# Optimization experiments

Measured on AMD Instinct MI355X. Metric: run time of the kernel, lower is better.

Reference implementation:

```python
import jax, jax.numpy as jnp
import numpy as np

N_SAMPLES, N_ASSETS = 64, 256
N_CLUSTERS, N_INIT, MAX_ITER = 8, 10, 30
SEED = 42


def cov2corr(cov):
    d = jnp.sqrt(jnp.diagonal(cov, axis1=-2, axis2=-1))
    return cov / (d[..., :, None] * d[..., None, :])


def kmeans_single(x, key):
    # x: (n, d) points; Lloyd's algorithm, 'random' init (pick n_clusters points).
    n = x.shape[0]
    idx = jax.random.choice(key, n, (N_CLUSTERS,), replace=False)
    centers0 = x[idx]

    def step(centers, _):
        d2 = ((x[:, None, :] - centers[None, :, :]) ** 2).sum(-1)  # (n, k)
        ixs = jnp.argmin(d2, axis=1)
        onehot = jax.nn.one_hot(ixs, N_CLUSTERS, dtype=x.dtype)    # (n, k)
        counts = onehot.sum(0)
        new_centers = (onehot.T @ x) / jnp.maximum(counts, 1.0)[:, None]
        new_centers = jnp.where(counts[:, None] > 0, new_centers, centers)
        return new_centers, None

    centers, _ = jax.lax.scan(step, centers0, None, length=MAX_ITER)
    d2 = ((x[:, None, :] - centers[None, :, :]) ** 2).sum(-1)
    ixs = jnp.argmin(d2, axis=1)
    inertia = jnp.min(d2, axis=1).sum()
    return ixs, inertia


def cluster_weights(mask, cov, r):
    # Masked-block analytical Markowitz: solving the system with identity on the
    # off-cluster block and zero RHS is exactly the sub-matrix solve of the original.
    n = cov.shape[0]
    eye = jnp.eye(n, dtype=cov.dtype)
    m2 = mask[:, None] & mask[None, :]
    A = jnp.where(m2, cov, eye)
    b = jnp.where(mask, r, 0.0)
    w = jnp.linalg.solve(A, b)          # zeros outside cluster by construction
    denom = w.sum()                     # = ones^T Sigma_c^{-1} mu_c
    return jnp.where(denom != 0, w / denom, 0.0)


def nco_sample(cov, r, key):
    corr = cov2corr(cov)
    keys = jax.random.split(key, N_INIT)
    ixs_all, inertia = jax.vmap(lambda k: kmeans_single(corr, k))(keys)
    ixs = jax.lax.stop_gradient(ixs_all[jnp.argmin(inertia)])      # (n,)
    masks = ixs[None, :] == jnp.arange(N_CLUSTERS)[:, None]        # (k, n)
    w_cols = jax.vmap(cluster_weights, in_axes=(0, None, None))(masks, cov, r)  # (k, n)
    w_intra = w_cols.T                                             # (n, k)
    inter_cov = w_intra.T @ cov @ w_intra                          # (k, k)
    inter_rets = w_intra.T @ r                                     # (k,)
    w_u = jnp.linalg.solve(inter_cov, inter_rets)
    w_inter = w_u / w_u.sum()
    return w_intra @ w_inter                                       # (n,)


def setup_inputs() -> dict:
    key = jax.random.key(0)
    k1, k2 = jax.random.split(key)
    # SPD covariance: factor model + diagonal jitter
    F = jax.random.normal(k1, (N_SAMPLES, N_ASSETS, N_ASSETS), dtype=jnp.float32)
    covmat = jnp.einsum('bij,bkj->bik', F, F) / N_ASSETS \
        + 0.1 * jnp.eye(N_ASSETS, dtype=jnp.float32)[None]
    rets = jax.random.uniform(k2, (N_SAMPLES, N_ASSETS), dtype=jnp.float32,
                              minval=0.01, maxval=1.0)
    return {"covmat": covmat, "rets": rets}


def reference(covmat, rets):
    base = jax.random.key(SEED)
    keys = jax.random.split(base, covmat.shape[0])
    return jax.vmap(nco_sample)(covmat, rets, keys)  # (n_samples, n_assets)
```

## Files before the change

### kernel.cpp

```cpp
#include <hip/hip_runtime.h>
#include <stdint.h>

#define NS 64
#define NA 256
#define NC 8
#define NI 10
#define MAXIT 30
#define MSMALL 64
#define MLDS 132

typedef unsigned int u32;
typedef unsigned long long u64;

struct Key { u32 x, y; };

__device__ __forceinline__ void tf2x32(u32 k0, u32 k1, u32 c0, u32 c1, u32& o0, u32& o1) {
  u32 ks0 = k0, ks1 = k1, ks2 = k0 ^ k1 ^ 0x1BD11BDAu;
  u32 x0 = c0 + ks0, x1 = c1 + ks1;
#define TFR(r) { x0 += x1; x1 = (x1 << (r)) | (x1 >> (32 - (r))); x1 ^= x0; }
  TFR(13) TFR(15) TFR(26) TFR(6)
  x0 += ks1; x1 += ks2 + 1u;
  TFR(17) TFR(29) TFR(16) TFR(24)
  x0 += ks2; x1 += ks0 + 2u;
  TFR(13) TFR(15) TFR(26) TFR(6)
  x0 += ks0; x1 += ks1 + 3u;
  TFR(17) TFR(29) TFR(16) TFR(24)
  x0 += ks1; x1 += ks2 + 4u;
  TFR(13) TFR(15) TFR(26) TFR(6)
  x0 += ks2; x1 += ks0 + 5u;
#undef TFR
  o0 = x0; o1 = x1;
}

__device__ __forceinline__ Key key_row(Key k, u32 j) {
  Key r; tf2x32(k.x, k.y, 0u, j, r.x, r.y); return r;
}
__device__ __forceinline__ u32 rbits32(Key k, u32 i) {
  u32 o0, o1; tf2x32(k.x, k.y, 0u, i, o0, o1); return o0 ^ o1;
}

__global__ __launch_bounds__(256) void nco_gram_kernel(
    const float* __restrict__ cov, double* __restrict__ G) {
  int b = blockIdx.x;
  int j = b / 10, tile = b - 10 * j;
  const int TIa[10] = {0,0,0,0,1,1,1,2,2,3};
  const int TJa[10] = {0,1,2,3,1,2,3,2,3,3};
  int ti2 = TIa[tile], tj2 = TJa[tile];
  const float* C = cov + (size_t)j * NA * NA;
  double* Gj = G + (size_t)j * NA * NA;

  __shared__ double sinv[NA];
  __shared__ double As[16][64 + 1];
  __shared__ double Bs[16][64 + 1];
  int t = threadIdx.x;
  int tr = t >> 4, tc = t & 15;

  sinv[t] = 1.0 / sqrt((double)C[(size_t)t * NA + t]);
  __syncthreads();

  double acc[4][4];
#pragma unroll
  for (int a = 0; a < 4; a++)
#pragma unroll
    for (int bb = 0; bb < 4; bb++) acc[a][bb] = 0.0;

  for (int k0 = 0; k0 < NA; k0 += 16) {
    int kk = t & 15, rr = t >> 4;
    double ck = sinv[k0 + kk];
#pragma unroll
    for (int m = 0; m < 4; m++) {
      int r = rr + 16 * m;
      int gr = ti2 * 64 + r;
      As[kk][r] = (double)C[(size_t)gr * NA + k0 + kk] * sinv[gr] * ck;
      int gc = tj2 * 64 + r;
      Bs[kk][r] = (double)C[(size_t)gc * NA + k0 + kk] * sinv[gc] * ck;
    }
    __syncthreads();
#pragma unroll
    for (int kk2 = 0; kk2 < 16; kk2++) {
      double ar[4], br[4];
#pragma unroll
      for (int m = 0; m < 4; m++) ar[m] = As[kk2][tr + 16 * m];
#pragma unroll
      for (int m = 0; m < 4; m++) br[m] = Bs[kk2][tc + 16 * m];
#pragma unroll
      for (int a = 0; a < 4; a++)
#pragma unroll
        for (int bb = 0; bb < 4; bb++) acc[a][bb] = fma(ar[a], br[bb], acc[a][bb]);
    }
    __syncthreads();
  }
#pragma unroll
  for (int a = 0; a < 4; a++) {
    int gr = ti2 * 64 + tr + 16 * a;
#pragma unroll
    for (int bb = 0; bb < 4; bb++) {
      int gc = tj2 * 64 + tc + 16 * bb;
      Gj[(size_t)gr * NA + gc] = acc[a][bb];
      if (ti2 != tj2) Gj[(size_t)gc * NA + gr] = acc[a][bb];
    }
  }
}

__global__ __launch_bounds__(512) void nco_kmeans_kernel(
    const double* __restrict__ G, int* __restrict__ ixsAll,
    double* __restrict__ inertiaAll) {
  int b = blockIdx.x;
  int xcd = b & 7, s0 = b >> 3;
  int j  = xcd + 8 * (s0 / NI);
  int mi = s0 - (s0 / NI) * NI;
  int blk = j * NI + mi;
  int tid = threadIdx.x;
  int t = tid & 255;
  int g = tid >> 8;
  int w4 = tid >> 6;
  const double* Gj = G + (size_t)j * NA * NA;

  __shared__ int    li[NC][NA];
  __shared__ double sv[NC][NA];
  __shared__ int    wcnt[4][NC];
  __shared__ u64    balPrev[4][NC];
  __shared__ u64    balNew[4][NC];
  __shared__ u64    dAdd[4][NC];
  __shared__ u64    dRem[4][NC];
  __shared__ int    nsz[NC];
  __shared__ int    dirty[NC];
  __shared__ double part[NC][8];
  __shared__ double sinvn[NC], ck2[NC];
  __shared__ u32    bits[NA];

  if (g == 0) {
    Key base; base.x = 0u; base.y = 42u;
    Key skey = key_row(base, (u32)j);
    Key ikey = key_row(skey, (u32)mi);
    Key sub  = key_row(ikey, 1u);
    bits[t] = rbits32(sub, (u32)t);
  }
  __syncthreads();
  if (g == 0) {
    u32 mine = bits[t];
    int rank = 0;
    for (int u = 0; u < NA; u++) {
      u32 b2 = bits[u];
      rank += (b2 < mine) || (b2 == mine && u < t);
    }
    if (rank < NC) li[rank][0] = t;
    if (t < NC) { nsz[t] = 1; dirty[t] = 1; }
#pragma unroll
    for (int k = 0; k < NC; k++) {
      u64 bal = __ballot(rank == k);
      if ((t & 63) == 0) balPrev[w4][k] = bal;
    }
  }
  __syncthreads();

  double xx = (g == 0) ? Gj[(size_t)t * NA + t] : 0.0;
  int myix = -1;
  double fb = 0.0;
  for (int it = 0; it <= MAXIT; ++it) {
    if (it > 0) {
      u64 mybal = 0;
      if (g == 0) {
#pragma unroll
        for (int k = 0; k < NC; k++) {
          u64 bal = __ballot(myix == k);
          if ((t & 63) == 0) { wcnt[w4][k] = (int)__popcll(bal); balNew[w4][k] = bal; }
          if (k == myix) mybal = bal;
        }
      }
      __syncthreads();
      if (g == 0) {
        if (t < NC) {
          int tot = wcnt[0][t] + wcnt[1][t] + wcnt[2][t] + wcnt[3][t];
          if (tot > 0) {
            nsz[t] = tot;
            bool d = (balNew[0][t] != balPrev[0][t]) | (balNew[1][t] != balPrev[1][t]) |
                     (balNew[2][t] != balPrev[2][t]) | (balNew[3][t] != balPrev[3][t]);
            dirty[t] = d ? 1 : 0;
            if (d) {
#pragma unroll
              for (int w2 = 0; w2 < 4; w2++) {
                dAdd[w2][t] = balNew[w2][t] & ~balPrev[w2][t];
                dRem[w2][t] = balPrev[w2][t] & ~balNew[w2][t];
                balPrev[w2][t] = balNew[w2][t];
              }
            }
          } else {
            dirty[t] = 0;
          }
        }
        int k = myix;
        int base = 0;
        for (int w2 = 0; w2 < w4; w2++) base += wcnt[w2][k];
        li[k][base + (int)__popcll(mybal & ((1ULL << (t & 63)) - 1ULL))] = t;
      }
      __syncthreads();
      if (!(dirty[0] | dirty[1] | dirty[2] | dirty[3] |
            dirty[4] | dirty[5] | dirty[6] | dirty[7])) break;

      for (int k = g; k < NC; k += 2) {
        if (!dirty[k]) continue;
        if (it == 1) {
          int n = nsz[k];
          const int* lk = li[k];
          double a0 = 0.0, a1 = 0.0;
          int i = 0;
          for (; i + 4 <= n; i += 4) {
            int r0 = lk[i], r1 = lk[i + 1], r2 = lk[i + 2], r3 = lk[i + 3];
            double g0 = Gj[(size_t)r0 * NA + t];
            double g1 = Gj[(size_t)r1 * NA + t];
            double g2 = Gj[(size_t)r2 * NA + t];
            double g3 = Gj[(size_t)r3 * NA + t];
            a0 += g0; a1 += g1; a0 += g2; a1 += g3;
          }
          for (; i < n; ++i) a0 += Gj[(size_t)lk[i] * NA + t];
          sv[k][t] = a0 + a1;
        } else {
          double acc = sv[k][t];
#pragma unroll
          for (int wq = 0; wq < 4; wq++) {
            u64 m0 = dRem[wq][k];
            while (m0) {
              int p = (wq << 6) + (int)__builtin_ctzll(m0);
              m0 &= m0 - 1;
              acc -= Gj[(size_t)p * NA + t];
            }
          }
#pragma unroll
          for (int wq = 0; wq < 4; wq++) {
            u64 m0 = dAdd[wq][k];
            while (m0) {
              int p = (wq << 6) + (int)__builtin_ctzll(m0);
              m0 &= m0 - 1;
              acc += Gj[(size_t)p * NA + t];
            }
          }
          sv[k][t] = acc;
        }
      }
    } else {
      for (int k = g; k < NC; k += 2) {
        int p = li[k][0];
        sv[k][t] = Gj[(size_t)p * NA + t];
      }
    }
    __syncthreads();

    if (tid < 64) {
      int k = tid >> 3, r = tid & 7;
      if (dirty[k]) {
        int n = nsz[k];
        double p = 0.0;
        for (int i = r; i < n; i += 8) p += sv[k][li[k][i]];
        part[k][r] = p;
      }
      __builtin_amdgcn_wave_barrier();
      if (tid < NC && dirty[tid]) {
        double S = 0.0;
#pragma unroll
        for (int r2 = 0; r2 < 8; r2++) S += part[tid][r2];
        double inn = 1.0 / (double)nsz[tid];
        sinvn[tid] = inn;
        ck2[tid] = S * inn * inn;
      }
    }
    __syncthreads();

    if (g == 0) {
      double best = ck2[0] - 2.0 * sv[0][t] * sinvn[0]; int bi = 0;
#pragma unroll
      for (int k = 1; k < NC; k++) {
        double f = ck2[k] - 2.0 * sv[k][t] * sinvn[k];
        if (f < best) { best = f; bi = k; }
      }
      fb = best;
      myix = bi;
    }
  }

  __syncthreads();
  double* red = (double*)&li[0][0];
  if (g == 0) red[t] = xx + fb;
  __syncthreads();
  if (g == 0) ixsAll[blk * NA + t] = myix;
  if (tid == 0) {
    double ss = 0.0;
    for (int i = 0; i < NA; i++) ss += red[i];
    inertiaAll[blk] = ss;
  }
}

__global__ __launch_bounds__(256) void nco_csolve_small(
    const float* __restrict__ cov, const float* __restrict__ rets,
    const int* __restrict__ ixsAll, const double* __restrict__ inertiaAll,
    double* __restrict__ wc_all) {
  int b = blockIdx.x;
  int j = b >> 3, c = b & 7;
  int t = threadIdx.x, w = t >> 6;
  const float* C = cov + (size_t)j * NA * NA;
  const float* r = rets + (size_t)j * NA;

  __shared__ double bufl[MSMALL * (MSMALL + 1)];
  __shared__ double prow[MSMALL];
  __shared__ int    li[NA];
  __shared__ int    wcnt[4][NC];
  __shared__ int    scnt[NC];
  __shared__ int    sbest;
  __shared__ double rhs[NA];
  __shared__ double wsub[NA];

  if (t == 0) {
    double bv = inertiaAll[j * NI]; int bb = 0;
    for (int m = 1; m < NI; m++) {
      double v = inertiaAll[j * NI + m];
      if (v < bv) { bv = v; bb = m; }
    }
    sbest = bb;
  }
  __syncthreads();
  const int* ixs = ixsAll + (size_t)(j * NI + sbest) * NA;

  int myc = ixs[t];
  u64 mybal = 0;
#pragma unroll
  for (int u = 0; u < NC; u++) {
    u64 bal = __ballot(myc == u);
    if ((t & 63) == 0) wcnt[w][u] = (int)__popcll(bal);
    if (u == myc) mybal = bal;
  }
  __syncthreads();
  if (t < NC) scnt[t] = wcnt[0][t] + wcnt[1][t] + wcnt[2][t] + wcnt[3][t];
  __syncthreads();
  if (myc == c) {
    int base = 0;
    for (int w2 = 0; w2 < w; w2++) base += wcnt[w2][c];
    li[base + (int)__popcll(mybal & ((1ULL << (t & 63)) - 1ULL))] = t;
  }
  __syncthreads();

  int m = scnt[c];
  if (m > MSMALL) return;

  double* wcc = wc_all + ((size_t)j * NC + c) * NA;
  wcc[t] = 0.0;
  if (m == 0) return;

  int ms = m | 1;
  for (int idx = t; idx < m * m; idx += NA) {
    int row = idx / m, col = idx - row * m;
    bufl[row * ms + col] = (double)C[(size_t)li[row] * NA + li[col]];
  }
  if (t < m) rhs[t] = (double)r[li[t]];
  __syncthreads();
  if (t < 64) {
    for (int k = 0; k < m - 1; k++) {
      for (int q = k + 1 + t; q < m; q += 64) prow[q] = bufl[k * ms + q];
      __builtin_amdgcn_wave_barrier();
      double piv = bufl[k * ms + k];
      if (t > k && t < m) {
        double f = bufl[t * ms + k] / piv;
        rhs[t] -= f * rhs[k];
        for (int b2 = k + 1; b2 < m; b2++)
          bufl[t * ms + b2] -= f * prow[b2];
      }
      __builtin_amdgcn_wave_barrier();
    }
    for (int a = m - 1; a >= 0; a--) {
      if (t == a) wsub[a] = rhs[a] / bufl[a * ms + a];
      __builtin_amdgcn_wave_barrier();
      if (t < a) rhs[t] -= bufl[t * ms + a] * wsub[a];
      __builtin_amdgcn_wave_barrier();
    }
    double ssum = 0.0;
    for (int a = 0; a < m; a++) ssum += wsub[a];
    if (t < m) wcc[li[t]] = (ssum != 0.0) ? (wsub[t] / ssum) : 0.0;
  }
}

__global__ __launch_bounds__(512) void nco_csolve_large(
    const float* __restrict__ cov, const float* __restrict__ rets,
    const int* __restrict__ ixsAll, const double* __restrict__ inertiaAll,
    double* __restrict__ gbuf_all, double* __restrict__ wc_all) {
  int b = blockIdx.x;
  int j = b >> 3, c = b & 7;
  int tid = threadIdx.x;
  int t = tid & 255, w = t >> 6;
  const float* C = cov + (size_t)j * NA * NA;
  const float* r = rets + (size_t)j * NA;

  __shared__ double bufl[MLDS * (MLDS + 1)];
  __shared__ double prowL[NA];
  __shared__ int    li[NA];
  __shared__ int    wcnt[4][NC];
  __shared__ int    scnt[NC];
  __shared__ int    sbest;
  __shared__ double rhs[NA];
  __shared__ double wsub[NA];
  __shared__ double fv[NA];

  if (tid == 0) {
    double bv = inertiaAll[j * NI]; int bb = 0;
    for (int m = 1; m < NI; m++) {
      double v = inertiaAll[j * NI + m];
      if (v < bv) { bv = v; bb = m; }
    }
    sbest = bb;
  }
  __syncthreads();
  const int* ixs = ixsAll + (size_t)(j * NI + sbest) * NA;

  int myc = (tid < 256) ? ixs[t] : -1;
  u64 mybal = 0;
#pragma unroll
  for (int u = 0; u < NC; u++) {
    u64 bal = __ballot(myc == u);
    if (tid < 256 && (t & 63) == 0) wcnt[w][u] = (int)__popcll(bal);
    if (u == myc) mybal = bal;
  }
  __syncthreads();
  if (tid < NC) scnt[tid] = wcnt[0][tid] + wcnt[1][tid] + wcnt[2][tid] + wcnt[3][tid];
  __syncthreads();
  if (tid < 256 && myc == c) {
    int base = 0;
    for (int w2 = 0; w2 < w; w2++) base += wcnt[w2][c];
    li[base + (int)__popcll(mybal & ((1ULL << (t & 63)) - 1ULL))] = t;
  }
  __syncthreads();

  int m = scnt[c];
  if (m <= MSMALL) return;

  double* wcc = wc_all + ((size_t)j * NC + c) * NA;
  if (tid < 256) wcc[tid] = 0.0;

  int inlds = (m <= MLDS);
  int msl = inlds ? (m | 1) : m;
  double* bp = inlds ? bufl : ({
    int soff = 0;
    for (int u = 0; u < c; u++) soff += scnt[u] * scnt[u];
    gbuf_all + (size_t)j * NA * NA + soff; });

  for (int idx = tid; idx < m * m; idx += 512) {
    int row = idx / m, col = idx - row * m;
    bp[(size_t)row * msl + col] = (double)C[(size_t)li[row] * NA + li[col]];
  }
  if (tid < m) rhs[tid] = (double)r[li[tid]];
  __syncthreads();

  for (int k = 0; k < m - 1; k++) {
    double piv = bp[(size_t)k * msl + k];
    int nr = m - 1 - k;
    if (tid < nr) {
      int row = k + 1 + tid;
      double f = bp[(size_t)row * msl + k] / piv;
      fv[row] = f;
      rhs[row] -= f * rhs[k];
    }
    for (int q = k + 1 + tid; q < m; q += 512) prowL[q] = bp[(size_t)k * msl + q];
    __syncthreads();
    int tot = nr * nr;
    for (int idx = tid; idx < tot; idx += 512) {
      int rr = idx / nr, cc = idx - rr * nr;
      int row = k + 1 + rr, col = k + 1 + cc;
      bp[(size_t)row * msl + col] -= fv[row] * prowL[col];
    }
    __syncthreads();
  }

  if (tid < 64) {
    for (int a = m - 1; a >= 0; a--) {
      if ((a & 63) == tid) wsub[a] = rhs[a] / bp[(size_t)a * msl + a];
      __builtin_amdgcn_wave_barrier();
      for (int r2 = tid; r2 < a; r2 += 64) rhs[r2] -= bp[(size_t)r2 * msl + a] * wsub[a];
      __builtin_amdgcn_wave_barrier();
    }
    double ssum = 0.0;
    for (int a = 0; a < m; a++) ssum += wsub[a];
    for (int r2 = tid; r2 < m; r2 += 64)
      wcc[li[r2]] = (ssum != 0.0) ? (wsub[r2] / ssum) : 0.0;
  }
}

__global__ __launch_bounds__(256) void nco_inter_kernel(
    const float* __restrict__ cov, const float* __restrict__ rets,
    const double* __restrict__ wc_all, float* __restrict__ out) {
  int j = blockIdx.x, t = threadIdx.x;
  const float* C = cov + (size_t)j * NA * NA;
  const float* r = rets + (size_t)j * NA;

  __shared__ double wc[NC][NA];
  __shared__ double tmpL[NC][NA];
  __shared__ double interA[NC][NC];
  __shared__ double interb[NC];
  __shared__ double wi[NC];

  for (int c = 0; c < NC; c++) wc[c][t] = wc_all[((size_t)j * NC + c) * NA + t];
  __syncthreads();

  {
    double tcol[NC];
#pragma unroll
    for (int c = 0; c < NC; c++) tcol[c] = 0.0;
    for (int p = 0; p < NA; p++) {
      double cv = (double)C[(size_t)p * NA + t];
#pragma unroll
      for (int c = 0; c < NC; c++) tcol[c] += wc[c][p] * cv;
    }
#pragma unroll
    for (int c = 0; c < NC; c++) tmpL[c][t] = tcol[c];
  }
  __syncthreads();

  if (t < NC * NC) {
    int c = t / NC, c2 = t % NC;
    double s = 0.0;
    for (int q = 0; q < NA; q++) s += tmpL[c][q] * wc[c2][q];
    interA[c][c2] = s;
  }
  if (t >= 64 && t < 64 + NC) {
    int c = t - 64;
    double s = 0.0;
    for (int p = 0; p < NA; p++) s += wc[c][p] * (double)r[p];
    interb[c] = s;
  }
  __syncthreads();

  if (t == 0) {
    double A[NC][NC], bb[NC];
    for (int a = 0; a < NC; a++) {
      bb[a] = interb[a];
      for (int q = 0; q < NC; q++) A[a][q] = interA[a][q];
    }
    for (int k = 0; k < NC; k++) {
      int p = k; double mx = fabs(A[k][k]);
      for (int i2 = k + 1; i2 < NC; i2++) {
        double v = fabs(A[i2][k]);
        if (v > mx) { mx = v; p = i2; }
      }
      if (p != k) {
        for (int q = 0; q < NC; q++) { double tv = A[k][q]; A[k][q] = A[p][q]; A[p][q] = tv; }
        double tb = bb[k]; bb[k] = bb[p]; bb[p] = tb;
      }
      for (int i2 = k + 1; i2 < NC; i2++) {
        double f = A[i2][k] / A[k][k];
        bb[i2] -= f * bb[k];
        for (int q = k + 1; q < NC; q++) A[i2][q] -= f * A[k][q];
      }
    }
    double w[NC];
    for (int a = NC - 1; a >= 0; a--) {
      double s = bb[a];
      for (int q = a + 1; q < NC; q++) s -= A[a][q] * w[q];
      w[a] = s / A[a][a];
    }
    double ssum = 0.0;
    for (int a = 0; a < NC; a++) ssum += w[a];
    for (int a = 0; a < NC; a++) wi[a] = w[a] / ssum;
  }
  __syncthreads();

  double o = 0.0;
#pragma unroll
  for (int c = 0; c < NC; c++) o += wc[c][t] * wi[c];
  out[(size_t)j * NA + t] = (float)o;
}

extern "C" void kernel_launch(void* const* d_in, const int* in_sizes, int n_in,
                              void* d_out, int out_size, void* d_ws, size_t ws_size,
                              hipStream_t stream) {
  const float* cov  = (const float*)d_in[0];
  const float* rets = (const float*)d_in[1];
  float* out = (float*)d_out;
  char* ws = (char*)d_ws;

  const size_t g_bytes = (size_t)NS * NA * NA * sizeof(double);
  double* G          = (double*)(ws);
  double* inertiaAll = (double*)(ws + g_bytes);
  int*    ixsAll     = (int*)   (ws + g_bytes + 5120);
  double* wc_all     = (double*)(ws + g_bytes + 5120 + 655360);
  double* gbuf_all   = G;

  hipLaunchKernelGGL(nco_gram_kernel,   dim3(NS * 10), dim3(NA),  0, stream, cov, G);
  hipLaunchKernelGGL(nco_kmeans_kernel, dim3(NS * NI), dim3(512), 0, stream,
                     G, ixsAll, inertiaAll);
  hipLaunchKernelGGL(nco_csolve_small,  dim3(NS * NC), dim3(NA),  0, stream,
                     cov, rets, ixsAll, inertiaAll, wc_all);
  hipLaunchKernelGGL(nco_csolve_large,  dim3(NS * NC), dim3(512), 0, stream,
                     cov, rets, ixsAll, inertiaAll, gbuf_all, wc_all);
  hipLaunchKernelGGL(nco_inter_kernel,  dim3(NS),      dim3(NA),  0, stream,
                     cov, rets, wc_all, out);
}
```

Baseline: 275.3 us.

## Split inter-cluster kernel into per-cluster blocks plus final solve kernel

The single 64-block inter-cluster kernel is replaced by a 512-block kernel, one block per sample and cluster, that computes one row of w^T C w and the matching w^T r entry, followed by a small 64-block kernel that runs the 8x8 solve and forms the output. The aim is to fill more of the GPU during the covariance projection, which previously ran on only 64 blocks. In exchange, each covariance matrix is read eight times instead of once, and there is an extra kernel launch plus a round trip through global memory.

```diff
diff --git a/kernel.cpp b/kernel.cpp
--- a/kernel.cpp
+++ b/kernel.cpp
@@ -481,55 +481,53 @@
   }
 }
 
-__global__ __launch_bounds__(256) void nco_inter_kernel(
+__global__ __launch_bounds__(256) void nco_interA_kernel(
     const float* __restrict__ cov, const float* __restrict__ rets,
-    const double* __restrict__ wc_all, float* __restrict__ out) {
-  int j = blockIdx.x, t = threadIdx.x;
+    const double* __restrict__ wc_all,
+    double* __restrict__ interA_all, double* __restrict__ interb_all) {
+  int b = blockIdx.x;
+  int j = b >> 3, c = b & 7;
+  int t = threadIdx.x;
   const float* C = cov + (size_t)j * NA * NA;
   const float* r = rets + (size_t)j * NA;
 
-  __shared__ double wc[NC][NA];
-  __shared__ double tmpL[NC][NA];
-  __shared__ double interA[NC][NC];
-  __shared__ double interb[NC];
+  __shared__ double wcs[NC][NA];
+  __shared__ double tmpL[NA];
+
+  for (int cc = 0; cc < NC; cc++) wcs[cc][t] = wc_all[((size_t)j * NC + cc) * NA + t];
+  __syncthreads();
+
+  {
+    double s = 0.0;
+    for (int p = 0; p < NA; p++)
+      s += wcs[c][p] * (double)C[(size_t)p * NA + t];
+    tmpL[t] = s;
+  }
+  __syncthreads();
+
+  if (t < NC) {
+    double s = 0.0;
+    for (int q = 0; q < NA; q++) s += tmpL[q] * wcs[t][q];
+    interA_all[(size_t)j * NC * NC + c * NC + t] = s;
+  }
+  if (t == NC) {
+    double s = 0.0;
+    for (int p = 0; p < NA; p++) s += wcs[c][p] * (double)r[p];
+    interb_all[(size_t)j * NC + c] = s;
+  }
+}
+
+__global__ __launch_bounds__(256) void nco_final_kernel(
+    const double* __restrict__ wc_all, const double* __restrict__ interA_all,
+    const double* __restrict__ interb_all, float* __restrict__ out) {
+  int j = blockIdx.x, t = threadIdx.x;
   __shared__ double wi[NC];
-
-  for (int c = 0; c < NC; c++) wc[c][t] = wc_all[((size_t)j * NC + c) * NA + t];
-  __syncthreads();
-
-  {
-    double tcol[NC];
-#pragma unroll
-    for (int c = 0; c < NC; c++) tcol[c] = 0.0;
-    for (int p = 0; p < NA; p++) {
-      double cv = (double)C[(size_t)p * NA + t];
-#pragma unroll
-      for (int c = 0; c < NC; c++) tcol[c] += wc[c][p] * cv;
-    }
-#pragma unroll
-    for (int c = 0; c < NC; c++) tmpL[c][t] = tcol[c];
-  }
-  __syncthreads();
-
-  if (t < NC * NC) {
-    int c = t / NC, c2 = t % NC;
-    double s = 0.0;
-    for (int q = 0; q < NA; q++) s += tmpL[c][q] * wc[c2][q];
-    interA[c][c2] = s;
-  }
-  if (t >= 64 && t < 64 + NC) {
-    int c = t - 64;
-    double s = 0.0;
-    for (int p = 0; p < NA; p++) s += wc[c][p] * (double)r[p];
-    interb[c] = s;
-  }
-  __syncthreads();
 
   if (t == 0) {
     double A[NC][NC], bb[NC];
     for (int a = 0; a < NC; a++) {
-      bb[a] = interb[a];
-      for (int q = 0; q < NC; q++) A[a][q] = interA[a][q];
+      bb[a] = interb_all[(size_t)j * NC + a];
+      for (int q = 0; q < NC; q++) A[a][q] = interA_all[(size_t)j * NC * NC + a * NC + q];
     }
     for (int k = 0; k < NC; k++) {
       int p = k; double mx = fabs(A[k][k]);
@@ -561,7 +559,8 @@
 
   double o = 0.0;
 #pragma unroll
-  for (int c = 0; c < NC; c++) o += wc[c][t] * wi[c];
+  for (int c = 0; c < NC; c++)
+    o += wc_all[((size_t)j * NC + c) * NA + t] * wi[c];
   out[(size_t)j * NA + t] = (float)o;
 }
 
@@ -578,6 +577,8 @@
   double* inertiaAll = (double*)(ws + g_bytes);
   int*    ixsAll     = (int*)   (ws + g_bytes + 5120);
   double* wc_all     = (double*)(ws + g_bytes + 5120 + 655360);
+  double* interA_all = (double*)(ws + g_bytes + 5120 + 655360 + 1048576);
+  double* interb_all = (double*)(ws + g_bytes + 5120 + 655360 + 1048576 + 32768);
   double* gbuf_all   = G;
 
   hipLaunchKernelGGL(nco_gram_kernel,   dim3(NS * 10), dim3(NA),  0, stream, cov, G);
@@ -587,6 +588,8 @@
                      cov, rets, ixsAll, inertiaAll, wc_all);
   hipLaunchKernelGGL(nco_csolve_large,  dim3(NS * NC), dim3(512), 0, stream,
                      cov, rets, ixsAll, inertiaAll, gbuf_all, wc_all);
-  hipLaunchKernelGGL(nco_inter_kernel,  dim3(NS),      dim3(NA),  0, stream,
-                     cov, rets, wc_all, out);
-}
+  hipLaunchKernelGGL(nco_interA_kernel, dim3(NS * NC), dim3(NA),  0, stream,
+                     cov, rets, wc_all, interA_all, interb_all);
+  hipLaunchKernelGGL(nco_final_kernel,  dim3(NS),      dim3(NA),  0, stream,
+                     wc_all, interA_all, interb_all, out);
+}
```

Result: no change. 280.7 us (+1.9%).
